# Optimization experiments

Measured on AMD Instinct MI355X. Metric: run time of the kernel, lower is better.

Reference implementation:

```python
import jax, jax.numpy as jnp
import numpy as np

NUM_USERS = 100000
NUM_ITEMS = 50000
NUM_EDGES = 1000000
EMB_DIM = 64


def setup_inputs() -> dict:
    key = jax.random.key(0)
    k1, k2, k3, k4, k5, k6 = jax.random.split(key, 6)
    return {
        "user_emb": jax.random.normal(k1, (NUM_USERS, EMB_DIM), dtype=jnp.float32),
        "item_emb": jax.random.normal(k2, (NUM_ITEMS, EMB_DIM), dtype=jnp.float32),
        "u_sw": jax.random.uniform(k3, (NUM_USERS, 1), dtype=jnp.float32),
        "i_sw": jax.random.uniform(k4, (NUM_ITEMS, 1), dtype=jnp.float32),
        "edge_src_user": jax.random.randint(k5, (NUM_EDGES,), 0, NUM_USERS, dtype=jnp.int32),
        "edge_dst_item": jax.random.randint(k6, (NUM_EDGES,), 0, NUM_ITEMS, dtype=jnp.int32),
    }


def _segment_mean(feat_src, src_idx, dst_idx, num_dst, inv_deg):
    # gather source node features onto edges, sum-reduce at destinations, divide by degree
    s = jax.ops.segment_sum(feat_src[src_idx], dst_idx, num_segments=num_dst)
    return s * inv_deg


def reference(user_emb, item_emb, u_sw, i_sw, edge_src_user, edge_dst_item):
    ones = jnp.ones((edge_src_user.shape[0],), dtype=user_emb.dtype)
    deg_i = jax.ops.segment_sum(ones, edge_dst_item, num_segments=NUM_ITEMS)
    deg_u = jax.ops.segment_sum(ones, edge_src_user, num_segments=NUM_USERS)
    # DGL mean gives 0 for zero-degree nodes
    inv_deg_i = jnp.where(deg_i > 0, 1.0 / jnp.maximum(deg_i, 1.0), 0.0)[:, None]
    inv_deg_u = jnp.where(deg_u > 0, 1.0 / jnp.maximum(deg_u, 1.0), 0.0)[:, None]

    def one_round(u, i):
        # 'like': user -> item mean aggregation; 'rev_like': item -> user
        new_i = _segment_mean(u, edge_src_user, edge_dst_item, NUM_ITEMS, inv_deg_i)
        new_u = _segment_mean(i, edge_dst_item, edge_src_user, NUM_USERS, inv_deg_u)
        return new_u + u * u_sw, new_i + i * i_sw

    u, i = one_round(user_emb, item_emb)
    u, i = one_round(u, i)
    return (u, i)
```

## Files before the change

### kernel.cpp

```cpp
#include <hip/hip_runtime.h>

#define NU 100000
#define NI 50000
#define NE 1000000
#define D  64
#define NBI 196
#define NBU 391
#define NB_TOT (NBI + NBU)
#define CHUNK 4096

__device__ __forceinline__ unsigned short f2bf(float f) {
    unsigned int u = __float_as_uint(f);
    u += 0x7FFFu + ((u >> 16) & 1u);
    return (unsigned short)(u >> 16);
}
__device__ __forceinline__ float bf2f(unsigned short h) {
    return __uint_as_float(((unsigned int)h) << 16);
}

__global__ void k_tobf16_both(const float* __restrict__ uin, const float* __restrict__ iin,
                              unsigned short* __restrict__ ubf ) {
    int i = blockIdx.x * blockDim.x + threadIdx.x;
    const int NU4 = NU * D / 4;
    const int NT4 = (NU + NI) * D / 4;
    if (i < NT4) {
        float4 f = (i < NU4) ? ((const float4*)uin)[i] : ((const float4*)iin)[i - NU4];
        ushort4 h;
        h.x = f2bf(f.x); h.y = f2bf(f.y); h.z = f2bf(f.z); h.w = f2bf(f.w);
        ((ushort4*)ubf)[i] = h;
    }
}

__global__ void k_bhist(const int* __restrict__ esrc, const int* __restrict__ edst,
                        int* __restrict__ bcnt, int ne) {
    __shared__ int h[NB_TOT];
    for (int b = threadIdx.x; b < NB_TOT; b += blockDim.x) h[b] = 0;
    __syncthreads();
    int stride = gridDim.x * blockDim.x;
    for (int e = blockIdx.x * blockDim.x + threadIdx.x; e < ne; e += stride) {
        atomicAdd(&h[edst[e] >> 8], 1);
        atomicAdd(&h[NBI + (esrc[e] >> 8)], 1);
    }
    __syncthreads();
    for (int b = threadIdx.x; b < NB_TOT; b += blockDim.x) {
        int v = h[b];
        if (v) atomicAdd(&bcnt[b], v);
    }
}

__global__ void k_bscan_both(const int* __restrict__ bcnt,
                             int* __restrict__ bbase_i, int* __restrict__ gcur_i,
                             int* __restrict__ bbase_u, int* __restrict__ gcur_u) {
    __shared__ int s[512];
    int tid = threadIdx.x;
    const int* in = (blockIdx.x == 0) ? bcnt : bcnt + NBI;
    int nb        = (blockIdx.x == 0) ? NBI : NBU;
    int* bbase    = (blockIdx.x == 0) ? bbase_i : bbase_u;
    int* gcur     = (blockIdx.x == 0) ? gcur_i : gcur_u;
    int v = (tid < nb) ? in[tid] : 0;
    s[tid] = v;
    __syncthreads();
    for (int o = 1; o < 512; o <<= 1) {
        int t = (tid >= o) ? s[tid - o] : 0;
        __syncthreads();
        s[tid] += t;
        __syncthreads();
    }
    if (tid < nb) { int ex = s[tid] - v; bbase[tid] = ex; gcur[tid] = ex; }
    if (tid == 0) bbase[nb] = NE;
}

__global__ void k_part_both(const int* __restrict__ esrc, const int* __restrict__ edst,
                            int* __restrict__ gcur_i, int* __restrict__ gcur_u,
                            unsigned int* __restrict__ rec_i, unsigned int* __restrict__ rec_u) {
    __shared__ int cnt_i[NBI], gb_i[NBI], cnt_u[NBU], gb_u[NBU];
    int tid = threadIdx.x;
    for (int b = tid; b < NBI; b += 256) cnt_i[b] = 0;
    for (int b = tid; b < NBU; b += 256) cnt_u[b] = 0;
    __syncthreads();
    int base = blockIdx.x * CHUNK;
    int dd[16], uu[16], ki[16], ku[16];
#pragma unroll
    for (int k = 0; k < 16; k++) {
        int j = base + tid + k * 256;
        dd[k] = -1;
        if (j < NE) {
            dd[k] = edst[j]; uu[k] = esrc[j];
            ki[k] = atomicAdd(&cnt_i[dd[k] >> 8], 1);
            ku[k] = atomicAdd(&cnt_u[uu[k] >> 8], 1);
        }
    }
    __syncthreads();
    for (int b = tid; b < NBI; b += 256) { int v = cnt_i[b]; if (v) gb_i[b] = atomicAdd(&gcur_i[b], v); }
    for (int b = tid; b < NBU; b += 256) { int v = cnt_u[b]; if (v) gb_u[b] = atomicAdd(&gcur_u[b], v); }
    __syncthreads();
#pragma unroll
    for (int k = 0; k < 16; k++) {
        if (dd[k] >= 0) {
            rec_i[gb_i[dd[k] >> 8] + ki[k]] = ((unsigned int)(dd[k] & 255) << 17) | (unsigned int)uu[k];
            rec_u[gb_u[uu[k] >> 8] + ku[k]] = ((unsigned int)(uu[k] & 255) << 17) | (unsigned int)dd[k];
        }
    }
}

__global__ void k_local_both(const unsigned int* __restrict__ rec_i, const unsigned int* __restrict__ rec_u,
                             const int* __restrict__ bbase_i, const int* __restrict__ bbase_u,
                             int* __restrict__ rp_i, int* __restrict__ rp_u,
                             int* __restrict__ col_i, int* __restrict__ col_u) {
    __shared__ int cnt[256];
    __shared__ int off[256];
    int tid = threadIdx.x;
    int t = blockIdx.x;
    bool item = t < NBI;
    int b = item ? t : t - NBI;
    const unsigned int* rec = item ? rec_i : rec_u;
    const int* bb = item ? bbase_i : bbase_u;
    int* rp  = item ? rp_i : rp_u;
    int* col = item ? col_i : col_u;
    int nn   = item ? NI : NU;
    int beg = bb[b], end = bb[b + 1];
    cnt[tid] = 0;
    __syncthreads();
    for (int j = beg + tid; j < end; j += 256)
        atomicAdd(&cnt[rec[j] >> 17], 1);
    __syncthreads();
    int v = cnt[tid];
    off[tid] = v;
    __syncthreads();
    for (int o = 1; o < 256; o <<= 1) {
        int tv = (tid >= o) ? off[tid - o] : 0;
        __syncthreads();
        off[tid] += tv;
        __syncthreads();
    }
    int ex = off[tid] - v;
    int node = b * 256 + tid;
    if (node <= nn) rp[node] = beg + ex;
    cnt[tid] = ex;
    __syncthreads();
    for (int j = beg + tid; j < end; j += 256) {
        unsigned int r = rec[j];
        int p = atomicAdd(&cnt[r >> 17], 1);
        col[beg + p] = (int)(r & 0x1FFFF);
    }
}

__device__ __forceinline__ void agg_wave(const unsigned short* __restrict__ feat,
                                         const float* self, const float* __restrict__ sw,
                                         const int* __restrict__ rp, const int* __restrict__ cols,
                                         float* out, unsigned short* out_bf,
                                         int w, int sub, int li) {
    int beg = rp[w], end = rp[w + 1];
    float4 a0 = make_float4(0.f, 0.f, 0.f, 0.f);
    float4 a1 = make_float4(0.f, 0.f, 0.f, 0.f);
    for (int j0 = beg; j0 < end; j0 += 8) {
        int e0 = j0 + sub, e1 = e0 + 4;
        bool v0 = e0 < end, v1 = e1 < end;
        int c0 = 0, c1 = 0;
        if (v0) c0 = cols[e0];
        if (v1) c1 = cols[e1];
        ushort4 h0, h1;
        if (v0) h0 = *(const ushort4*)(feat + (size_t)c0 * D + li * 4);
        if (v1) h1 = *(const ushort4*)(feat + (size_t)c1 * D + li * 4);
        if (v0) { a0.x += bf2f(h0.x); a0.y += bf2f(h0.y); a0.z += bf2f(h0.z); a0.w += bf2f(h0.w); }
        if (v1) { a1.x += bf2f(h1.x); a1.y += bf2f(h1.y); a1.z += bf2f(h1.z); a1.w += bf2f(h1.w); }
    }
    a0.x += a1.x; a0.y += a1.y; a0.z += a1.z; a0.w += a1.w;
    a0.x += __shfl_xor(a0.x, 16); a0.y += __shfl_xor(a0.y, 16);
    a0.z += __shfl_xor(a0.z, 16); a0.w += __shfl_xor(a0.w, 16);
    a0.x += __shfl_xor(a0.x, 32); a0.y += __shfl_xor(a0.y, 32);
    a0.z += __shfl_xor(a0.z, 32); a0.w += __shfl_xor(a0.w, 32);
    if (sub == 0) {
        int dgr = end - beg;
        float inv = (dgr > 0) ? (1.0f / (float)dgr) : 0.0f;
        float swv = sw[w];
        float4 s = *(const float4*)(self + (size_t)w * D + li * 4);
        float4 r;
        r.x = a0.x * inv + s.x * swv;
        r.y = a0.y * inv + s.y * swv;
        r.z = a0.z * inv + s.z * swv;
        r.w = a0.w * inv + s.w * swv;
        *(float4*)(out + (size_t)w * D + li * 4) = r;
        if (out_bf) {
            ushort4 hb;
            hb.x = f2bf(r.x); hb.y = f2bf(r.y); hb.z = f2bf(r.z); hb.w = f2bf(r.w);
            *(ushort4*)(out_bf + (size_t)w * D + li * 4) = hb;
        }
    }
}

__global__ void k_agg_bf(const unsigned short* __restrict__ feat, const float* self,
                         const float* __restrict__ sw, const int* __restrict__ rp,
                         const int* __restrict__ cols, float* out,
                         unsigned short* out_bf, int n_dst) {
    int w = (blockIdx.x * blockDim.x + threadIdx.x) >> 6;
    if (w >= n_dst) return;
    agg_wave(feat, self, sw, rp, cols, out, out_bf, w, (threadIdx.x >> 4) & 3, threadIdx.x & 15);
}

__global__ void k_agg2(const unsigned short* __restrict__ u1_bf, const unsigned short* __restrict__ i1_bf,
                       const float* __restrict__ i_sw, const float* __restrict__ u_sw,
                       const int* __restrict__ rp_i, const int* __restrict__ rp_u,
                       const int* __restrict__ col_i, const int* __restrict__ col_u,
                       float* out_i, float* out_u) {
    int w = (blockIdx.x * blockDim.x + threadIdx.x) >> 6;
    int sub = (threadIdx.x >> 4) & 3;
    int li  = threadIdx.x & 15;
    if (w < NI)
        agg_wave(u1_bf, out_i, i_sw, rp_i, col_i, out_i, nullptr, w, sub, li);
    else if (w < NI + NU)
        agg_wave(i1_bf, out_u, u_sw, rp_u, col_u, out_u, nullptr, w - NI, sub, li);
}

extern "C" void kernel_launch(void* const* d_in, const int* in_sizes, int n_in,
                              void* d_out, int out_size, void* d_ws, size_t ws_size,
                              hipStream_t stream) {
    const float* user_emb = (const float*)d_in[0];
    const float* item_emb = (const float*)d_in[1];
    const float* u_sw     = (const float*)d_in[2];
    const float* i_sw     = (const float*)d_in[3];
    const int*   esrc     = (const int*)d_in[4];
    const int*   edst     = (const int*)d_in[5];

    float* out_u = (float*)d_out;
    float* out_i = out_u + NU * D;

    int* bcnt    = (int*)d_ws;
    int* bbase_i = bcnt + NB_TOT;
    int* bbase_u = bbase_i + NBI + 1;
    int* gcur_i  = bbase_u + NBU + 1;
    int* gcur_u  = gcur_i + NBI;
    int* rp_i    = gcur_u + NBU;
    int* rp_u    = rp_i + NI + 1;
    int* col_i   = rp_u + NU + 1;
    int* col_u   = col_i + NE;
    uintptr_t pa = ((uintptr_t)(col_u + NE) + 15) & ~(uintptr_t)15;
    unsigned int* rec_i = (unsigned int*)pa;
    unsigned int* rec_u = rec_i + NE;
    unsigned short* i1_bf = (unsigned short*)rec_i;
    unsigned short* u_bf  = (unsigned short*)(rec_u + NE);
    unsigned short* u1_bf = u_bf;
    unsigned short* i_bf  = u_bf + (size_t)NU * D;

    hipMemsetAsync(bcnt, 0, NB_TOT * sizeof(int), stream);

    const int B = 256;

    k_bhist<<<512, B, 0, stream>>>(esrc, edst, bcnt, NE);
    k_bscan_both<<<2, 512, 0, stream>>>(bcnt, bbase_i, gcur_i, bbase_u, gcur_u);
    k_part_both<<<(NE + CHUNK - 1) / CHUNK, B, 0, stream>>>(esrc, edst, gcur_i, gcur_u, rec_i, rec_u);
    k_local_both<<<NB_TOT, B, 0, stream>>>(rec_i, rec_u, bbase_i, bbase_u, rp_i, rp_u, col_i, col_u);

    k_tobf16_both<<<((NU + NI) * D / 4 + B - 1) / B, B, 0, stream>>>(user_emb, item_emb, u_bf);

    int gi = (NI + 3) / 4;
    int gu = (NU + 3) / 4;

    k_agg_bf<<<gi, B, 0, stream>>>(u_bf, item_emb, i_sw, rp_i, col_i, out_i, i1_bf, NI);
    k_agg_bf<<<gu, B, 0, stream>>>(i_bf, user_emb, u_sw, rp_u, col_u, out_u, u1_bf, NU);

    k_agg2<<<(NI + NU + 3) / 4, B, 0, stream>>>(u1_bf, i1_bf, i_sw, u_sw,
                                                rp_i, rp_u, col_i, col_u, out_i, out_u);
}
```

Before: 337.4 us.

## Use 16-lane groups per node with shuffled column indices; drop bf16 preconversion pass

Result: faster. 278.2 us (-17.5%).

```diff
diff --git a/kernel.cpp b/kernel.cpp
--- a/kernel.cpp
+++ b/kernel.cpp
@@ -16,19 +16,6 @@
 }
 __device__ __forceinline__ float bf2f(unsigned short h) {
     return __uint_as_float(((unsigned int)h) << 16);
-}
-
-__global__ void k_tobf16_both(const float* __restrict__ uin, const float* __restrict__ iin,
-                              unsigned short* __restrict__ ubf ) {
-    int i = blockIdx.x * blockDim.x + threadIdx.x;
-    const int NU4 = NU * D / 4;
-    const int NT4 = (NU + NI) * D / 4;
-    if (i < NT4) {
-        float4 f = (i < NU4) ? ((const float4*)uin)[i] : ((const float4*)iin)[i - NU4];
-        ushort4 h;
-        h.x = f2bf(f.x); h.y = f2bf(f.y); h.z = f2bf(f.z); h.w = f2bf(f.w);
-        ((ushort4*)ubf)[i] = h;
-    }
 }
 
 __global__ void k_bhist(const int* __restrict__ esrc, const int* __restrict__ edst,
@@ -145,71 +132,123 @@
     }
 }
 
-__device__ __forceinline__ void agg_wave(const unsigned short* __restrict__ feat,
-                                         const float* self, const float* __restrict__ sw,
-                                         const int* __restrict__ rp, const int* __restrict__ cols,
-                                         float* out, unsigned short* out_bf,
-                                         int w, int sub, int li) {
-    int beg = rp[w], end = rp[w + 1];
-    float4 a0 = make_float4(0.f, 0.f, 0.f, 0.f);
-    float4 a1 = make_float4(0.f, 0.f, 0.f, 0.f);
-    for (int j0 = beg; j0 < end; j0 += 8) {
-        int e0 = j0 + sub, e1 = e0 + 4;
-        bool v0 = e0 < end, v1 = e1 < end;
-        int c0 = 0, c1 = 0;
-        if (v0) c0 = cols[e0];
-        if (v1) c1 = cols[e1];
-        ushort4 h0, h1;
-        if (v0) h0 = *(const ushort4*)(feat + (size_t)c0 * D + li * 4);
-        if (v1) h1 = *(const ushort4*)(feat + (size_t)c1 * D + li * 4);
-        if (v0) { a0.x += bf2f(h0.x); a0.y += bf2f(h0.y); a0.z += bf2f(h0.z); a0.w += bf2f(h0.w); }
-        if (v1) { a1.x += bf2f(h1.x); a1.y += bf2f(h1.y); a1.z += bf2f(h1.z); a1.w += bf2f(h1.w); }
-    }
-    a0.x += a1.x; a0.y += a1.y; a0.z += a1.z; a0.w += a1.w;
-    a0.x += __shfl_xor(a0.x, 16); a0.y += __shfl_xor(a0.y, 16);
-    a0.z += __shfl_xor(a0.z, 16); a0.w += __shfl_xor(a0.w, 16);
-    a0.x += __shfl_xor(a0.x, 32); a0.y += __shfl_xor(a0.y, 32);
-    a0.z += __shfl_xor(a0.z, 32); a0.w += __shfl_xor(a0.w, 32);
-    if (sub == 0) {
-        int dgr = end - beg;
-        float inv = (dgr > 0) ? (1.0f / (float)dgr) : 0.0f;
-        float swv = sw[w];
-        float4 s = *(const float4*)(self + (size_t)w * D + li * 4);
-        float4 r;
-        r.x = a0.x * inv + s.x * swv;
-        r.y = a0.y * inv + s.y * swv;
-        r.z = a0.z * inv + s.z * swv;
-        r.w = a0.w * inv + s.w * swv;
-        *(float4*)(out + (size_t)w * D + li * 4) = r;
-        if (out_bf) {
-            ushort4 hb;
-            hb.x = f2bf(r.x); hb.y = f2bf(r.y); hb.z = f2bf(r.z); hb.w = f2bf(r.w);
-            *(ushort4*)(out_bf + (size_t)w * D + li * 4) = hb;
-        }
-    }
-}
-
-__global__ void k_agg_bf(const unsigned short* __restrict__ feat, const float* self,
-                         const float* __restrict__ sw, const int* __restrict__ rp,
-                         const int* __restrict__ cols, float* out,
-                         unsigned short* out_bf, int n_dst) {
-    int w = (blockIdx.x * blockDim.x + threadIdx.x) >> 6;
-    if (w >= n_dst) return;
-    agg_wave(feat, self, sw, rp, cols, out, out_bf, w, (threadIdx.x >> 4) & 3, threadIdx.x & 15);
-}
-
-__global__ void k_agg2(const unsigned short* __restrict__ u1_bf, const unsigned short* __restrict__ i1_bf,
-                       const float* __restrict__ i_sw, const float* __restrict__ u_sw,
-                       const int* __restrict__ rp_i, const int* __restrict__ rp_u,
-                       const int* __restrict__ col_i, const int* __restrict__ col_u,
-                       float* out_i, float* out_u) {
-    int w = (blockIdx.x * blockDim.x + threadIdx.x) >> 6;
-    int sub = (threadIdx.x >> 4) & 3;
-    int li  = threadIdx.x & 15;
-    if (w < NI)
-        agg_wave(u1_bf, out_i, i_sw, rp_i, col_i, out_i, nullptr, w, sub, li);
-    else if (w < NI + NU)
-        agg_wave(i1_bf, out_u, u_sw, rp_u, col_u, out_u, nullptr, w - NI, sub, li);
+__device__ __forceinline__ void agg_g_f32(const float* __restrict__ feat,
+        const float* __restrict__ self, const float* __restrict__ sw,
+        const int* __restrict__ rp, const int* __restrict__ cols,
+        float* __restrict__ out, unsigned short* __restrict__ out_bf,
+        int n, int li, int lb) {
+    int beg = rp[n], end = rp[n + 1];
+    float4 a = make_float4(0.f, 0.f, 0.f, 0.f);
+    for (int j0 = beg; j0 < end; j0 += 16) {
+        int cv = (j0 + li < end) ? cols[j0 + li] : 0;
+        int nj = end - j0; if (nj > 16) nj = 16;
+        int j = 0;
+        for (; j + 4 <= nj; j += 4) {
+            int c0 = __shfl(cv, lb + j,     64);
+            int c1 = __shfl(cv, lb + j + 1, 64);
+            int c2 = __shfl(cv, lb + j + 2, 64);
+            int c3 = __shfl(cv, lb + j + 3, 64);
+            float4 f0 = *(const float4*)(feat + (size_t)c0 * D + li * 4);
+            float4 f1 = *(const float4*)(feat + (size_t)c1 * D + li * 4);
+            float4 f2 = *(const float4*)(feat + (size_t)c2 * D + li * 4);
+            float4 f3 = *(const float4*)(feat + (size_t)c3 * D + li * 4);
+            a.x += f0.x + f1.x + f2.x + f3.x;
+            a.y += f0.y + f1.y + f2.y + f3.y;
+            a.z += f0.z + f1.z + f2.z + f3.z;
+            a.w += f0.w + f1.w + f2.w + f3.w;
+        }
+        for (; j < nj; ++j) {
+            int c = __shfl(cv, lb + j, 64);
+            float4 f = *(const float4*)(feat + (size_t)c * D + li * 4);
+            a.x += f.x; a.y += f.y; a.z += f.z; a.w += f.w;
+        }
+    }
+    int dgr = end - beg;
+    float inv = (dgr > 0) ? (1.0f / (float)dgr) : 0.0f;
+    float swv = sw[n];
+    float4 s = *(const float4*)(self + (size_t)n * D + li * 4);
+    float4 r;
+    r.x = a.x * inv + s.x * swv;
+    r.y = a.y * inv + s.y * swv;
+    r.z = a.z * inv + s.z * swv;
+    r.w = a.w * inv + s.w * swv;
+    *(float4*)(out + (size_t)n * D + li * 4) = r;
+    if (out_bf) {
+        ushort4 hb;
+        hb.x = f2bf(r.x); hb.y = f2bf(r.y); hb.z = f2bf(r.z); hb.w = f2bf(r.w);
+        *(ushort4*)(out_bf + (size_t)n * D + li * 4) = hb;
+    }
+}
+
+__device__ __forceinline__ void agg_g_bf(const unsigned short* __restrict__ feat,
+        const float* __restrict__ self, const float* __restrict__ sw,
+        const int* __restrict__ rp, const int* __restrict__ cols,
+        float* __restrict__ out, int n, int li, int lb) {
+    int beg = rp[n], end = rp[n + 1];
+    float4 a = make_float4(0.f, 0.f, 0.f, 0.f);
+    for (int j0 = beg; j0 < end; j0 += 16) {
+        int cv = (j0 + li < end) ? cols[j0 + li] : 0;
+        int nj = end - j0; if (nj > 16) nj = 16;
+        int j = 0;
+        for (; j + 4 <= nj; j += 4) {
+            int c0 = __shfl(cv, lb + j,     64);
+            int c1 = __shfl(cv, lb + j + 1, 64);
+            int c2 = __shfl(cv, lb + j + 2, 64);
+            int c3 = __shfl(cv, lb + j + 3, 64);
+            ushort4 h0 = *(const ushort4*)(feat + (size_t)c0 * D + li * 4);
+            ushort4 h1 = *(const ushort4*)(feat + (size_t)c1 * D + li * 4);
+            ushort4 h2 = *(const ushort4*)(feat + (size_t)c2 * D + li * 4);
+            ushort4 h3 = *(const ushort4*)(feat + (size_t)c3 * D + li * 4);
+            a.x += bf2f(h0.x) + bf2f(h1.x) + bf2f(h2.x) + bf2f(h3.x);
+            a.y += bf2f(h0.y) + bf2f(h1.y) + bf2f(h2.y) + bf2f(h3.y);
+            a.z += bf2f(h0.z) + bf2f(h1.z) + bf2f(h2.z) + bf2f(h3.z);
+            a.w += bf2f(h0.w) + bf2f(h1.w) + bf2f(h2.w) + bf2f(h3.w);
+        }
+        for (; j < nj; ++j) {
+            int c = __shfl(cv, lb + j, 64);
+            ushort4 h = *(const ushort4*)(feat + (size_t)c * D + li * 4);
+            a.x += bf2f(h.x); a.y += bf2f(h.y); a.z += bf2f(h.z); a.w += bf2f(h.w);
+        }
+    }
+    int dgr = end - beg;
+    float inv = (dgr > 0) ? (1.0f / (float)dgr) : 0.0f;
+    float swv = sw[n];
+    float4 s = *(const float4*)(self + (size_t)n * D + li * 4);
+    float4 r;
+    r.x = a.x * inv + s.x * swv;
+    r.y = a.y * inv + s.y * swv;
+    r.z = a.z * inv + s.z * swv;
+    r.w = a.w * inv + s.w * swv;
+    *(float4*)(out + (size_t)n * D + li * 4) = r;
+}
+
+__global__ void k_agg_r1(const float* __restrict__ user_emb, const float* __restrict__ item_emb,
+                         const float* __restrict__ u_sw, const float* __restrict__ i_sw,
+                         const int* __restrict__ rp_i, const int* __restrict__ rp_u,
+                         const int* __restrict__ col_i, const int* __restrict__ col_u,
+                         float* out_i, float* out_u,
+                         unsigned short* i1_bf, unsigned short* u1_bf) {
+    int g  = (blockIdx.x * blockDim.x + threadIdx.x) >> 4;
+    int li = threadIdx.x & 15;
+    int lb = threadIdx.x & 48;
+    if (g < NI)
+        agg_g_f32(user_emb, item_emb, i_sw, rp_i, col_i, out_i, i1_bf, g, li, lb);
+    else if (g < NI + NU)
+        agg_g_f32(item_emb, user_emb, u_sw, rp_u, col_u, out_u, u1_bf, g - NI, li, lb);
+}
+
+__global__ void k_agg_r2(const unsigned short* __restrict__ u1_bf, const unsigned short* __restrict__ i1_bf,
+                         const float* __restrict__ u_sw, const float* __restrict__ i_sw,
+                         const int* __restrict__ rp_i, const int* __restrict__ rp_u,
+                         const int* __restrict__ col_i, const int* __restrict__ col_u,
+                         float* out_i, float* out_u) {
+    int g  = (blockIdx.x * blockDim.x + threadIdx.x) >> 4;
+    int li = threadIdx.x & 15;
+    int lb = threadIdx.x & 48;
+    if (g < NI)
+        agg_g_bf(u1_bf, out_i, i_sw, rp_i, col_i, out_i, g, li, lb);
+    else if (g < NI + NU)
+        agg_g_bf(i1_bf, out_u, u_sw, rp_u, col_u, out_u, g - NI, li, lb);
 }
 
 extern "C" void kernel_launch(void* const* d_in, const int* in_sizes, int n_in,
@@ -235,12 +274,10 @@
     int* col_i   = rp_u + NU + 1;
     int* col_u   = col_i + NE;
     uintptr_t pa = ((uintptr_t)(col_u + NE) + 15) & ~(uintptr_t)15;
+    unsigned short* u1_bf = (unsigned short*)pa;
+    unsigned short* i1_bf = u1_bf + (size_t)NU * D;
     unsigned int* rec_i = (unsigned int*)pa;
     unsigned int* rec_u = rec_i + NE;
-    unsigned short* i1_bf = (unsigned short*)rec_i;
-    unsigned short* u_bf  = (unsigned short*)(rec_u + NE);
-    unsigned short* u1_bf = u_bf;
-    unsigned short* i_bf  = u_bf + (size_t)NU * D;
 
     hipMemsetAsync(bcnt, 0, NB_TOT * sizeof(int), stream);
 
@@ -251,14 +288,12 @@
     k_part_both<<<(NE + CHUNK - 1) / CHUNK, B, 0, stream>>>(esrc, edst, gcur_i, gcur_u, rec_i, rec_u);
     k_local_both<<<NB_TOT, B, 0, stream>>>(rec_i, rec_u, bbase_i, bbase_u, rp_i, rp_u, col_i, col_u);
 
-    k_tobf16_both<<<((NU + NI) * D / 4 + B - 1) / B, B, 0, stream>>>(user_emb, item_emb, u_bf);
-
-    int gi = (NI + 3) / 4;
-    int gu = (NU + 3) / 4;
-
-    k_agg_bf<<<gi, B, 0, stream>>>(u_bf, item_emb, i_sw, rp_i, col_i, out_i, i1_bf, NI);
-    k_agg_bf<<<gu, B, 0, stream>>>(i_bf, user_emb, u_sw, rp_u, col_u, out_u, u1_bf, NU);
-
-    k_agg2<<<(NI + NU + 3) / 4, B, 0, stream>>>(u1_bf, i1_bf, i_sw, u_sw,
-                                                rp_i, rp_u, col_i, col_u, out_i, out_u);
-}
+    int gblocks = ((NI + NU) * 16 + B - 1) / B;
+
+    k_agg_r1<<<gblocks, B, 0, stream>>>(user_emb, item_emb, u_sw, i_sw,
+                                        rp_i, rp_u, col_i, col_u,
+                                        out_i, out_u, i1_bf, u1_bf);
+    k_agg_r2<<<gblocks, B, 0, stream>>>(u1_bf, i1_bf, u_sw, i_sw,
+                                        rp_i, rp_u, col_i, col_u,
+                                        out_i, out_u);
+}
```
